# Kernel tuning notes

Measured on AMD Instinct MI355X. Metric: run time of the kernel, lower is better.

## Reference

```python
import jax, jax.numpy as jnp
import numpy as np

DIM = 512
HEADS = 8
DIM_HEAD = 64          # dim // 8
M = 256                # num_landmarks = dim // 2
PINV_ITERS = 6
SCALE = DIM_HEAD ** -0.5
KERNEL = 33            # residual_conv_kernel


def setup_inputs() -> dict:
    key = jax.random.key(0)
    ks = jax.random.split(key, 5)
    b, n = 4, 4096  # n divisible by M -> no padding branch
    inner = HEADS * DIM_HEAD
    x = jax.random.normal(ks[0], (b, n, DIM), jnp.float32)
    ln_w = jnp.ones((DIM,), jnp.float32)
    ln_b = jnp.zeros((DIM,), jnp.float32)
    w_qkv = jax.random.normal(ks[1], (DIM, 3 * inner), jnp.float32) / np.sqrt(DIM)
    w_out = jax.random.normal(ks[2], (inner, DIM), jnp.float32) / np.sqrt(inner)
    b_out = jnp.zeros((DIM,), jnp.float32)
    # depthwise Conv2d(heads, heads, (33,1), groups=heads, bias=False): weight [H,1,33,1]
    w_res = jax.random.normal(ks[3], (HEADS, 1, KERNEL, 1), jnp.float32) * 0.05
    return dict(x=x, ln_w=ln_w, ln_b=ln_b, w_qkv=w_qkv, w_out=w_out, b_out=b_out, w_res=w_res)


def moore_penrose_iter_pinv(x, iters=PINV_ITERS):
    # x: (..., m, m) row-stochastic softmax matrix
    abs_x = jnp.abs(x)
    col = abs_x.sum(-1).max()   # global max, matches torch.max(col)
    row = abs_x.sum(-2).max()
    z = jnp.swapaxes(x, -1, -2) / (col * row)
    I = jnp.eye(x.shape[-1], dtype=x.dtype)
    for _ in range(iters):
        xz = x @ z
        z = 0.25 * z @ (13 * I - xz @ (15 * I - xz @ (7 * I - xz)))
    return z


def reference(x, ln_w, ln_b, w_qkv, w_out, b_out, w_res):
    b, n, d = x.shape
    # pre-norm LayerNorm (eps=1e-5, biased variance)
    mu = x.mean(-1, keepdims=True)
    var = ((x - mu) ** 2).mean(-1, keepdims=True)
    h = (x - mu) * jax.lax.rsqrt(var + 1e-5) * ln_w + ln_b

    qkv = h @ w_qkv                           # (b, n, 3*inner)
    q, k, v = jnp.split(qkv, 3, axis=-1)
    to_heads = lambda t: t.reshape(b, n, HEADS, DIM_HEAD).transpose(0, 2, 1, 3)
    q = to_heads(q) * SCALE                   # (b, h, n, d)
    k = to_heads(k)
    v = to_heads(v)

    # landmarks: mean over consecutive chunks of size l = n // M
    l = n // M
    q_l = q.reshape(b, HEADS, M, l, DIM_HEAD).mean(3)  # (b, h, m, d)
    k_l = k.reshape(b, HEADS, M, l, DIM_HEAD).mean(3)

    sim1 = jnp.einsum('bhid,bhjd->bhij', q, k_l)       # (b, h, n, m)
    sim2 = jnp.einsum('bhid,bhjd->bhij', q_l, k_l)     # (b, h, m, m)
    sim3 = jnp.einsum('bhid,bhjd->bhij', q_l, k)       # (b, h, m, n)
    attn1 = jax.nn.softmax(sim1, -1)
    attn2 = jax.nn.softmax(sim2, -1)
    attn3 = jax.nn.softmax(sim3, -1)

    attn2_inv = moore_penrose_iter_pinv(attn2)
    out = (attn1 @ attn2_inv) @ (attn3 @ v)            # (b, h, n, d)

    # residual depthwise conv over sequence dim, per head
    pad = KERNEL // 2
    res = jax.lax.conv_general_dilated(
        v, w_res, window_strides=(1, 1), padding=((pad, pad), (0, 0)),
        dimension_numbers=('NCHW', 'OIHW', 'NCHW'), feature_group_count=HEADS)
    out = out + res

    out = out.transpose(0, 2, 1, 3).reshape(b, n, HEADS * DIM_HEAD)
    out = out @ w_out + b_out                          # to_out (dropout=identity in eval)
    return x + out
```

## Files before the change

kernel.cpp:

```cpp
#include <hip/hip_runtime.h>
#include <hip/hip_bf16.h>
#include <hip/hip_fp16.h>

#define B_ 4
#define H_ 8
#define N_ 4096
#define DH_ 64
#define D_ 512
#define M_ 256
#define BH_ 32
#define NT_ 16384

typedef unsigned short u16;
using sh8 = __attribute__((ext_vector_type(8))) short;
using sh4 = __attribute__((ext_vector_type(4))) short;
using f4  = __attribute__((ext_vector_type(4))) float;

__device__ __forceinline__ float bf2f(u16 u){ return __uint_as_float(((unsigned)u)<<16); }
__device__ __forceinline__ u16 f2bf(float f){
  unsigned u = __float_as_uint(f);
  u += 0x7fffu + ((u>>16)&1u);
  return (u16)(u>>16);
}

__global__ __launch_bounds__(256) void ln_kernel(const float* __restrict__ x,
    const float* __restrict__ w, const float* __restrict__ b, u16* __restrict__ h){
  int row = blockIdx.x;
  const float2* xr = (const float2*)(x + (size_t)row*D_);
  int t = threadIdx.x;
  float2 v = xr[t];
  float s = v.x+v.y, ss = v.x*v.x+v.y*v.y;
  #pragma unroll
  for (int o=32;o;o>>=1){ s += __shfl_xor(s,o); ss += __shfl_xor(ss,o); }
  __shared__ float sb[4], sb2[4];
  if ((t&63)==0){ sb[t>>6]=s; sb2[t>>6]=ss; }
  __syncthreads();
  float ts  = sb[0]+sb[1]+sb[2]+sb[3];
  float tss = sb2[0]+sb2[1]+sb2[2]+sb2[3];
  float mean = ts*(1.f/D_);
  float var  = tss*(1.f/D_) - mean*mean;
  float rstd = rsqrtf(var+1e-5f);
  int c = 2*t;
  float o0 = (v.x-mean)*rstd*w[c]   + b[c];
  float o1 = (v.y-mean)*rstd*w[c+1] + b[c+1];
  u16* hr = h + (size_t)row*D_;
  hr[c] = f2bf(o0); hr[c+1] = f2bf(o1);
}

__global__ void castT2_kernel(const float* __restrict__ wqkv, u16* __restrict__ wqkvT,
    const float* __restrict__ wout, u16* __restrict__ woutT){
  int idx = blockIdx.x*256 + threadIdx.x;
  if (idx < 512*1536){
    int k = idx/1536, n = idx - k*1536;
    wqkvT[(size_t)n*512 + k] = f2bf(wqkv[idx]);
  } else {
    int i2 = idx - 512*1536;
    if (i2 < 512*512){
      int k = i2>>9, n = i2&511;
      woutT[(size_t)n*512 + k] = f2bf(wout[i2]);
    }
  }
}

__global__ __launch_bounds__(256) void gemm_qkv(const u16* __restrict__ A,
    const u16* __restrict__ Bt, u16* __restrict__ q, u16* __restrict__ k, u16* __restrict__ v){
  __shared__ short As[128*72], Bs[128*72];
  int r0 = blockIdx.x*128, c0 = blockIdx.y*128;
  int tid = threadIdx.x, lane = tid&63, w = tid>>6;
  int wr = w>>1, wc = w&1;
  f4 acc[4][4];
  #pragma unroll
  for (int i=0;i<4;i++){
    #pragma unroll
    for (int j=0;j<4;j++) acc[i][j]=0;
  }
  for (int kt=0;kt<8;kt++){
    __syncthreads();
    #pragma unroll
    for (int i=0;i<4;i++){
      int c = i*256+tid, row = c>>3, kg = c&7;
      *(sh8*)&As[row*72+kg*8] = *(const sh8*)(A + (size_t)(r0+row)*512 + kt*64 + kg*8);
      *(sh8*)&Bs[row*72+kg*8] = *(const sh8*)(Bt + (size_t)(c0+row)*512 + kt*64 + kg*8);
    }
    __syncthreads();
    #pragma unroll
    for (int kc=0;kc<2;kc++){
      sh8 a[4], bq[4];
      #pragma unroll
      for (int fr=0;fr<4;fr++) a[fr]  = *(const sh8*)&As[(wr*64+fr*16+(lane&15))*72 + kc*32 + ((lane>>4)<<3)];
      #pragma unroll
      for (int fc=0;fc<4;fc++) bq[fc] = *(const sh8*)&Bs[(wc*64+fc*16+(lane&15))*72 + kc*32 + ((lane>>4)<<3)];
      #pragma unroll
      for (int fr=0;fr<4;fr++){
        #pragma unroll
        for (int fc=0;fc<4;fc++)
          acc[fr][fc] = __builtin_amdgcn_mfma_f32_16x16x32_bf16(a[fr], bq[fc], acc[fr][fc], 0,0,0);
      }
    }
  }
  #pragma unroll
  for (int fr=0;fr<4;fr++){
    #pragma unroll
    for (int fc=0;fc<4;fc++){
      #pragma unroll
      for (int j=0;j<4;j++){
        int r = r0 + wr*64 + fr*16 + ((lane>>4)<<2) + j;
        int c = c0 + wc*64 + fc*16 + (lane&15);
        float val = acc[fr][fc][j];
        int which = c>>9, hh = (c>>6)&7, d = c&63;
        int bb = r>>12, n = r&4095;
        if (which==0) val *= 0.125f;
        u16* dst = which==0 ? q : (which==1 ? k : v);
        dst[(((size_t)(bb*8+hh))*4096 + n)*64 + d] = f2bf(val);
      }
    }
  }
}

__global__ __launch_bounds__(64) void landmark_kernel(const u16* __restrict__ q,
    const u16* __restrict__ k, u16* __restrict__ ql, u16* __restrict__ kl){
  int bh = blockIdx.x, m = blockIdx.y, d = threadIdx.x;
  const u16* qp = q + (((size_t)bh*4096) + m*16)*64 + d;
  const u16* kp = k + (((size_t)bh*4096) + m*16)*64 + d;
  float sq=0, sk=0;
  #pragma unroll
  for (int j=0;j<16;j++){ sq += bf2f(qp[j*64]); sk += bf2f(kp[j*64]); }
  ql[((size_t)bh*256+m)*64+d] = f2bf(sq*(1.f/16.f));
  kl[((size_t)bh*256+m)*64+d] = f2bf(sk*(1.f/16.f));
}

__global__ __launch_bounds__(256) void attn2_kernel(const u16* __restrict__ ql,
    const u16* __restrict__ kl, u16* __restrict__ Xhi, u16* __restrict__ Xlo){
  int bh = blockIdx.x, rb = blockIdx.y;
  __shared__ short klds[256*72];
  const u16* kg = kl + (size_t)bh*256*64;
  int tid = threadIdx.x;
  #pragma unroll
  for (int i=0;i<8;i++){
    int c = i*256+tid, row = c>>3, kgi = c&7;
    *(sh8*)&klds[row*72+kgi*8] = *(const sh8*)(kg + row*64 + kgi*8);
  }
  __syncthreads();
  int r = rb*16 + (tid>>4), t = tid&15;
  const u16* qr = ql + ((size_t)bh*256 + r)*64;
  float qv[64];
  #pragma unroll
  for (int i=0;i<8;i++){
    sh8 v8 = *(const sh8*)(qr + i*8);
    #pragma unroll
    for (int j=0;j<8;j++) qv[i*8+j] = bf2f((u16)v8[j]);
  }
  float s[16];
  #pragma unroll
  for (int j=0;j<16;j++){
    int col = t + 16*j;
    const short* kr = &klds[col*72];
    float accv=0;
    #pragma unroll
    for (int i8=0;i8<8;i8++){
      sh8 kv = *(const sh8*)(kr + i8*8);
      #pragma unroll
      for (int jj=0;jj<8;jj++) accv += qv[i8*8+jj]*bf2f((u16)kv[jj]);
    }
    s[j]=accv;
  }
  float mx = s[0];
  #pragma unroll
  for (int j=1;j<16;j++) mx = fmaxf(mx, s[j]);
  #pragma unroll
  for (int o=1;o<16;o<<=1) mx = fmaxf(mx, __shfl_xor(mx,o));
  float sum=0;
  #pragma unroll
  for (int j=0;j<16;j++){ s[j] = __expf(s[j]-mx); sum += s[j]; }
  #pragma unroll
  for (int o=1;o<16;o<<=1) sum += __shfl_xor(sum,o);
  float inv = 1.f/sum;
  u16* Xh = Xhi + ((size_t)bh*256 + r)*256;
  u16* Xl = Xlo + ((size_t)bh*256 + r)*256;
  #pragma unroll
  for (int j=0;j<16;j++){
    float val = s[j]*inv;
    u16 hb = f2bf(val);
    Xh[t+16*j] = hb; Xl[t+16*j] = f2bf(val - bf2f(hb));
  }
}

__global__ __launch_bounds__(256) void colrow_kernel(const u16* __restrict__ Xhi,
    const u16* __restrict__ Xlo, float* __restrict__ scal){
  int bh = blockIdx.x, t = threadIdx.x;
  const u16* xh = Xhi + (size_t)bh*65536;
  const u16* xl = Xlo + (size_t)bh*65536;
  float cs=0, rs=0;
  for (int m=0;m<256;m++) cs += bf2f(xh[m*256+t]) + bf2f(xl[m*256+t]);
  for (int c=0;c<256;c++) rs += bf2f(xh[t*256+c]) + bf2f(xl[t*256+c]);
  #pragma unroll
  for (int o=32;o;o>>=1){ cs = fmaxf(cs, __shfl_xor(cs,o)); rs = fmaxf(rs, __shfl_xor(rs,o)); }
  __shared__ float sb[4], sb2[4];
  if ((t&63)==0){ sb[t>>6]=cs; sb2[t>>6]=rs; }
  __syncthreads();
  if (t==0){
    float mc = fmaxf(fmaxf(sb[0],sb[1]),fmaxf(sb[2],sb[3]));
    float mr = fmaxf(fmaxf(sb2[0],sb2[1]),fmaxf(sb2[2],sb2[3]));
    atomicMax((unsigned*)&scal[1], __float_as_uint(mc));
    atomicMax((unsigned*)&scal[0], __float_as_uint(mr));
  }
}

__global__ __launch_bounds__(256) void ztinit_kernel(const u16* __restrict__ Xhi,
    const u16* __restrict__ Xlo, const float* __restrict__ scal,
    u16* __restrict__ Zhi, u16* __restrict__ Zlo, u16* __restrict__ ZThi, u16* __restrict__ ZTlo){
  int bh = blockIdx.x; int xr0 = blockIdx.y*64, xc0 = blockIdx.z*64;
  __shared__ float tb[64*66];
  float inv = 1.f/(scal[0]*scal[1]);
  int tid = threadIdx.x;
  size_t mo = (size_t)bh*65536;
  int row = tid>>2, cof = (tid&3)*16;
  #pragma unroll
  for (int s2=0;s2<2;s2++){
    sh8 hv = *(const sh8*)(Xhi + mo + (size_t)(xr0+row)*256 + xc0+cof+s2*8);
    sh8 lv = *(const sh8*)(Xlo + mo + (size_t)(xr0+row)*256 + xc0+cof+s2*8);
    #pragma unroll
    for (int j=0;j<8;j++) tb[row*66 + cof+s2*8+j] = (bf2f((u16)hv[j])+bf2f((u16)lv[j]))*inv;
  }
  __syncthreads();
  int lc = tid&63;
  #pragma unroll
  for (int i=0;i<16;i++){
    int lr = i*4 + (tid>>6);
    float v1 = tb[lr*66+lc];
    u16 h1 = f2bf(v1);
    ZThi[mo + (size_t)(xr0+lr)*256 + xc0+lc] = h1;
    ZTlo[mo + (size_t)(xr0+lr)*256 + xc0+lc] = f2bf(v1 - bf2f(h1));
    float v2 = tb[lc*66+lr];
    u16 h2 = f2bf(v2);
    Zhi[mo + (size_t)(xc0+lr)*256 + xr0+lc] = h2;
    Zlo[mo + (size_t)(xc0+lr)*256 + xr0+lc] = f2bf(v2 - bf2f(h2));
  }
}

__global__ __launch_bounds__(256) void pinv_mm(
    const u16* __restrict__ Ahi, const u16* __restrict__ Alo,
    const u16* __restrict__ Bthi, const u16* __restrict__ Btlo,
    u16* __restrict__ Chi, u16* __restrict__ Clo,
    u16* __restrict__ CThi, u16* __restrict__ CTlo,
    float beta, float alpha, int mode){
  int bh = blockIdx.z, r0 = blockIdx.x*64, c0 = blockIdx.y*64;
  size_t mo = (size_t)bh*65536;
  __shared__ __align__(16) short smem[2][4*2560];
  int tid=threadIdx.x, lane=tid&63, w=tid>>6, wr=w>>1, wc=w&1;
  int srow = tid>>2, skof = (tid&3)*8;
  const u16* pA  = Ahi  + mo + (size_t)(r0+srow)*256 + skof;
  const u16* pAl = Alo  + mo + (size_t)(r0+srow)*256 + skof;
  const u16* pB  = Bthi + mo + (size_t)(c0+srow)*256 + skof;
  const u16* pBl = Btlo + mo + (size_t)(c0+srow)*256 + skof;
  float av[2][2][4];
  if (mode){
    #pragma unroll
    for (int fr=0;fr<2;fr++){
      #pragma unroll
      for (int fc=0;fc<2;fc++){
        #pragma unroll
        for (int j=0;j<4;j++){
          int lr = wr*32+fr*16+((lane>>4)<<2)+j, lc = wc*32+fc*16+(lane&15);
          size_t o = mo+(size_t)(r0+lr)*256+c0+lc;
          av[fr][fc][j] = bf2f(Ahi[o]) + bf2f(Alo[o]);
        }
      }
    }
  }
  sh8 ra  = *(const sh8*)(pA);
  sh8 ral = *(const sh8*)(pAl);
  sh8 rb  = *(const sh8*)(pB);
  sh8 rbl = *(const sh8*)(pBl);
  f4 acc[2][2];
  #pragma unroll
  for (int i=0;i<2;i++){
    #pragma unroll
    for (int j=0;j<2;j++) acc[i][j]=0;
  }
  for (int kt=0;kt<8;kt++){
    short* Ah = &smem[kt&1][0];
    short* Al = Ah + 2560; short* Bh = Ah + 5120; short* Bl = Ah + 7680;
    *(sh8*)&Ah[srow*40+skof] = ra;
    *(sh8*)&Al[srow*40+skof] = ral;
    *(sh8*)&Bh[srow*40+skof] = rb;
    *(sh8*)&Bl[srow*40+skof] = rbl;
    __syncthreads();
    if (kt<7){
      int o2 = (kt+1)*32;
      ra  = *(const sh8*)(pA+o2);  ral = *(const sh8*)(pAl+o2);
      rb  = *(const sh8*)(pB+o2);  rbl = *(const sh8*)(pBl+o2);
    }
    sh8 ah[2], al[2], bh8[2], bl8[2];
    #pragma unroll
    for (int fr=0;fr<2;fr++){
      int off = (wr*32+fr*16+(lane&15))*40 + ((lane>>4)<<3);
      ah[fr] = *(const sh8*)&Ah[off]; al[fr] = *(const sh8*)&Al[off];
    }
    #pragma unroll
    for (int fc=0;fc<2;fc++){
      int off = (wc*32+fc*16+(lane&15))*40 + ((lane>>4)<<3);
      bh8[fc] = *(const sh8*)&Bh[off]; bl8[fc] = *(const sh8*)&Bl[off];
    }
    #pragma unroll
    for (int fr=0;fr<2;fr++){
      #pragma unroll
      for (int fc=0;fc<2;fc++){
        acc[fr][fc] = __builtin_amdgcn_mfma_f32_16x16x32_bf16(ah[fr], bh8[fc], acc[fr][fc], 0,0,0);
        acc[fr][fc] = __builtin_amdgcn_mfma_f32_16x16x32_bf16(ah[fr], bl8[fc], acc[fr][fc], 0,0,0);
        acc[fr][fc] = __builtin_amdgcn_mfma_f32_16x16x32_bf16(al[fr], bh8[fc], acc[fr][fc], 0,0,0);
      }
    }
  }
  __syncthreads();
  float* tb = (float*)&smem[0][0];
  #pragma unroll
  for (int fr=0;fr<2;fr++){
    #pragma unroll
    for (int fc=0;fc<2;fc++){
      #pragma unroll
      for (int j=0;j<4;j++){
        int lr = wr*32+fr*16+((lane>>4)<<2)+j, lc = wc*32+fc*16+(lane&15);
        float val = acc[fr][fc][j];
        if (mode) val = alpha*(beta*av[fr][fc][j] - val);
        tb[lr*66+lc] = val;
      }
    }
  }
  __syncthreads();
  int lc2 = tid&63;
  #pragma unroll
  for (int i=0;i<16;i++){
    int lr2 = i*4+(tid>>6);
    if (Chi){
      float v1 = tb[lr2*66+lc2];
      u16 hb=f2bf(v1);
      Chi[mo+(size_t)(r0+lr2)*256+c0+lc2]=hb;
      Clo[mo+(size_t)(r0+lr2)*256+c0+lc2]=f2bf(v1-bf2f(hb));
    }
    if (CThi){
      float v2 = tb[lc2*66 + lr2];
      u16 hb2=f2bf(v2);
      CThi[mo+(size_t)(c0+lr2)*256 + r0+lc2]=hb2;
      CTlo[mo+(size_t)(c0+lr2)*256 + r0+lc2]=f2bf(v2-bf2f(hb2));
    }
  }
}

__global__ __launch_bounds__(256) void gemm_logits(const u16* __restrict__ Aall,
    const u16* __restrict__ Btall, __half* __restrict__ Oall,
    int N, size_t sA, size_t sB, size_t sO){
  int bh = blockIdx.z;
  const u16* A  = Aall  + (size_t)bh*sA + (size_t)blockIdx.x*128*64;
  const u16* Bt = Btall + (size_t)bh*sB + (size_t)blockIdx.y*128*64;
  __half* O = Oall + (size_t)bh*sO + (size_t)blockIdx.x*128*N + (size_t)blockIdx.y*128;
  __shared__ short As[128*72], Bs[128*72];
  int tid=threadIdx.x, lane=tid&63, w=tid>>6, wr=w>>1, wc=w&1;
  #pragma unroll
  for (int i=0;i<4;i++){
    int c=i*256+tid, row=c>>3, kg=c&7;
    *(sh8*)&As[row*72+kg*8] = *(const sh8*)(A  + (size_t)row*64 + kg*8);
    *(sh8*)&Bs[row*72+kg*8] = *(const sh8*)(Bt + (size_t)row*64 + kg*8);
  }
  __syncthreads();
  f4 acc[4][4];
  #pragma unroll
  for (int i=0;i<4;i++){
    #pragma unroll
    for (int j=0;j<4;j++) acc[i][j]=0;
  }
  #pragma unroll
  for (int kc=0;kc<2;kc++){
    sh8 a[4], bq[4];
    #pragma unroll
    for (int fr=0;fr<4;fr++) a[fr]  = *(const sh8*)&As[(wr*64+fr*16+(lane&15))*72 + kc*32 + ((lane>>4)<<3)];
    #pragma unroll
    for (int fc=0;fc<4;fc++) bq[fc] = *(const sh8*)&Bs[(wc*64+fc*16+(lane&15))*72 + kc*32 + ((lane>>4)<<3)];
    #pragma unroll
    for (int fr=0;fr<4;fr++){
      #pragma unroll
      for (int fc=0;fc<4;fc++)
        acc[fr][fc] = __builtin_amdgcn_mfma_f32_16x16x32_bf16(a[fr], bq[fc], acc[fr][fc], 0,0,0);
    }
  }
  #pragma unroll
  for (int fr=0;fr<4;fr++){
    #pragma unroll
    for (int fc=0;fc<4;fc++){
      #pragma unroll
      for (int j=0;j<4;j++)
        O[(size_t)(wr*64+fr*16+((lane>>4)<<2)+j)*N + wc*64+fc*16+(lane&15)] = __float2half(acc[fr][fc][j]);
    }
  }
}

__global__ __launch_bounds__(256) void stats_kernel(const __half* __restrict__ logits,
    float2* __restrict__ stats, int RL){
  size_t row = blockIdx.x;
  const __half2* p = (const __half2*)(logits + row*RL);
  int t = threadIdx.x, n2 = RL>>1;
  float mx = -1e30f;
  for (int i=t;i<n2;i+=256){ float2 f = __half22float2(p[i]); mx = fmaxf(mx, fmaxf(f.x,f.y)); }
  #pragma unroll
  for (int o=32;o;o>>=1) mx = fmaxf(mx, __shfl_xor(mx,o));
  __shared__ float sb[4], sb2[4];
  if ((t&63)==0) sb[t>>6]=mx;
  __syncthreads();
  mx = fmaxf(fmaxf(sb[0],sb[1]),fmaxf(sb[2],sb[3]));
  float s=0;
  for (int i=t;i<n2;i+=256){ float2 f = __half22float2(p[i]); s += __expf(f.x-mx)+__expf(f.y-mx); }
  #pragma unroll
  for (int o=32;o;o>>=1) s += __shfl_xor(s,o);
  if ((t&63)==0) sb2[t>>6]=s;
  __syncthreads();
  s = sb2[0]+sb2[1]+sb2[2]+sb2[3];
  if (t==0) stats[row] = make_float2(mx, 1.f/s);
}

__global__ __launch_bounds__(256) void gemm_out3(const __half* __restrict__ Lall,
    const float2* __restrict__ stall, const u16* __restrict__ vall, float* __restrict__ part){
  int bh = blockIdx.z, mt = blockIdx.x, ks = blockIdx.y;
  const __half* L = Lall + (size_t)bh*256*4096 + (size_t)mt*128*4096 + (size_t)ks*512;
  const float2* st = stall + (size_t)bh*256 + mt*128;
  const u16* V = vall + (size_t)bh*4096*64 + (size_t)ks*512*64;
  float* O = part + ((size_t)(bh*8+ks)*256 + (size_t)mt*128)*64;
  __shared__ short As[128*72], Bs[64*72];
  int tid=threadIdx.x, lane=tid&63, w=tid>>6;
  f4 acc[2][4];
  #pragma unroll
  for (int i=0;i<2;i++){
    #pragma unroll
    for (int j=0;j<4;j++) acc[i][j]=0;
  }
  for (int kt=0;kt<8;kt++){
    __syncthreads();
    #pragma unroll
    for (int i=0;i<4;i++){
      int c=i*256+tid, row=c>>3, kg=c&7;
      const __half2* src = (const __half2*)(L + (size_t)row*4096 + kt*64 + kg*8);
      float2 ms = st[row];
      sh8 ov;
      #pragma unroll
      for (int jj=0;jj<4;jj++){
        float2 f = __half22float2(src[jj]);
        ov[2*jj]   = (short)f2bf(__expf(f.x-ms.x)*ms.y);
        ov[2*jj+1] = (short)f2bf(__expf(f.y-ms.x)*ms.y);
      }
      *(sh8*)&As[row*72+kg*8] = ov;
    }
    #pragma unroll
    for (int i=0;i<16;i++){
      int c=i*256+tid, d=c&63, nl=c>>6;
      Bs[d*72+nl] = (short)V[(size_t)(kt*64+nl)*64 + d];
    }
    __syncthreads();
    #pragma unroll
    for (int kc=0;kc<2;kc++){
      sh8 a[2], bq[4];
      #pragma unroll
      for (int fr=0;fr<2;fr++) a[fr]  = *(const sh8*)&As[(w*32+fr*16+(lane&15))*72 + kc*32+((lane>>4)<<3)];
      #pragma unroll
      for (int fc=0;fc<4;fc++) bq[fc] = *(const sh8*)&Bs[(fc*16+(lane&15))*72 + kc*32+((lane>>4)<<3)];
      #pragma unroll
      for (int fr=0;fr<2;fr++){
        #pragma unroll
        for (int fc=0;fc<4;fc++)
          acc[fr][fc] = __builtin_amdgcn_mfma_f32_16x16x32_bf16(a[fr], bq[fc], acc[fr][fc], 0,0,0);
      }
    }
  }
  #pragma unroll
  for (int fr=0;fr<2;fr++){
    #pragma unroll
    for (int fc=0;fc<4;fc++){
      #pragma unroll
      for (int j=0;j<4;j++)
        O[(size_t)(w*32+fr*16+((lane>>4)<<2)+j)*64 + fc*16+(lane&15)] = acc[fr][fc][j];
    }
  }
}

__global__ __launch_bounds__(256) void reduce_o3(const float* __restrict__ part, float* __restrict__ o3){
  int idx = blockIdx.x*256+threadIdx.x;
  int bh = idx>>14, rem = idx & 16383;
  float s=0;
  #pragma unroll
  for (int ks=0;ks<8;ks++) s += part[(((size_t)(bh*8+ks))<<14) + rem];
  o3[idx]=s;
}

__global__ __launch_bounds__(256) void wt_kernel(const u16* __restrict__ Zhi,
    const u16* __restrict__ Zlo, const float* __restrict__ o3, u16* __restrict__ Wt){
  int bh = blockIdx.x; int m = blockIdx.y*4 + (threadIdx.x>>6); int d = threadIdx.x&63;
  const u16* zh = Zhi + ((size_t)bh*256 + m)*256;
  const u16* zl = Zlo + ((size_t)bh*256 + m)*256;
  const float* op = o3 + (size_t)bh*256*64 + d;
  float accv = 0;
  for (int kk=0;kk<256;kk++) accv += (bf2f(zh[kk])+bf2f(zl[kk]))*op[kk*64];
  Wt[((size_t)bh*64 + d)*256 + m] = f2bf(accv);
}

__global__ __launch_bounds__(256) void fused_out1(const u16* __restrict__ q,
    const u16* __restrict__ klall, const u16* __restrict__ Wtall, float* __restrict__ Oall){
  int rb = blockIdx.x, bh = blockIdx.y;
  __shared__ __align__(16) short sm[18432];
  short* Bs = sm; short* P = sm;
  int tid=threadIdx.x, lane=tid&63, w=tid>>6;
  const u16* qb  = q + ((size_t)bh*4096 + (size_t)rb*64)*64;
  const u16* klb = klall + (size_t)bh*256*64;
  const u16* Wt  = Wtall + (size_t)bh*64*256;
  #pragma unroll
  for (int i=0;i<8;i++){
    int c = i*256+tid, row = c>>3, kg = c&7;
    *(sh8*)&Bs[row*72+kg*8] = *(const sh8*)(klb + row*64 + kg*8);
  }
  const u16* qrow = qb + (size_t)(w*16+(lane&15))*64 + ((lane>>4)<<3);
  sh8 a0 = *(const sh8*)(qrow);
  sh8 a1 = *(const sh8*)(qrow + 32);
  __syncthreads();
  f4 acc[16];
  #pragma unroll
  for (int fc=0;fc<16;fc++){
    sh8 b0 = *(const sh8*)&Bs[(fc*16+(lane&15))*72 + ((lane>>4)<<3)];
    sh8 b1 = *(const sh8*)&Bs[(fc*16+(lane&15))*72 + 32 + ((lane>>4)<<3)];
    acc[fc]=0;
    acc[fc] = __builtin_amdgcn_mfma_f32_16x16x32_bf16(a0, b0, acc[fc], 0,0,0);
    acc[fc] = __builtin_amdgcn_mfma_f32_16x16x32_bf16(a1, b1, acc[fc], 0,0,0);
  }
  float inv_[4];
  #pragma unroll
  for (int j=0;j<4;j++){
    float mx=-1e30f;
    #pragma unroll
    for (int fc=0;fc<16;fc++) mx = fmaxf(mx, acc[fc][j]);
    #pragma unroll
    for (int o=1;o<16;o<<=1) mx = fmaxf(mx, __shfl_xor(mx,o));
    float s=0;
    #pragma unroll
    for (int fc=0;fc<16;fc++){ float e=__expf(acc[fc][j]-mx); acc[fc][j]=e; s+=e; }
    #pragma unroll
    for (int o=1;o<16;o<<=1) s += __shfl_xor(s,o);
    inv_[j] = 1.f/s;
  }
  __syncthreads();
  #pragma unroll
  for (int fc=0;fc<16;fc++){
    #pragma unroll
    for (int j=0;j<4;j++){
      int row = w*16 + ((lane>>4)<<2) + j, col = fc*16 + (lane&15);
      P[row*268 + col] = (short)f2bf(acc[fc][j]*inv_[j]);
    }
  }
  __syncthreads();
  f4 acc2[4];
  #pragma unroll
  for (int fc2=0;fc2<4;fc2++) acc2[fc2]=0;
  #pragma unroll
  for (int kc=0;kc<8;kc++){
    sh8 a = *(const sh8*)&P[(w*16+(lane&15))*268 + kc*32 + ((lane>>4)<<3)];
    #pragma unroll
    for (int fc2=0;fc2<4;fc2++){
      int d = fc2*16 + (lane&15);
      sh8 b = *(const sh8*)(Wt + (size_t)d*256 + (kc*4+(lane>>4))*8);
      acc2[fc2] = __builtin_amdgcn_mfma_f32_16x16x32_bf16(a, b, acc2[fc2], 0,0,0);
    }
  }
  float* O = Oall + ((size_t)bh*4096 + (size_t)rb*64)*64;
  #pragma unroll
  for (int fc2=0;fc2<4;fc2++){
    #pragma unroll
    for (int j=0;j<4;j++){
      int row = w*16 + ((lane>>4)<<2)+j, col = fc2*16+(lane&15);
      O[(size_t)row*64 + col] = acc2[fc2][j];
    }
  }
}

__global__ __launch_bounds__(256) void combine_kernel(const float* __restrict__ out1,
    const u16* __restrict__ v, const float* __restrict__ wres, u16* __restrict__ oc){
  int bh = blockIdx.x; int hh = bh&7, bb = bh>>3;
  int n0 = blockIdx.y*64;
  int tid = threadIdx.x, d = tid&63, sub = tid>>6;
  int nbase = n0 + sub*16;
  const u16* vb = v + ((size_t)bh*4096)*64 + d;
  float w_[33];
  #pragma unroll
  for (int j=0;j<33;j++) w_[j] = wres[hh*33+j];
  float vv[48];
  #pragma unroll
  for (int i=0;i<48;i++){
    int nn = nbase + i - 16;
    vv[i] = (nn>=0 && nn<4096) ? bf2f(vb[(size_t)nn*64]) : 0.f;
  }
  #pragma unroll
  for (int r=0;r<16;r++){
    int n = nbase + r;
    float acc = out1[(((size_t)bh*4096)+n)*64 + d];
    #pragma unroll
    for (int j=0;j<33;j++) acc += w_[j]*vv[r+j];
    oc[((size_t)(bb*4096+n))*512 + hh*64 + d] = f2bf(acc);
  }
}

__global__ __launch_bounds__(256) void gemm_final(const u16* __restrict__ A,
    const u16* __restrict__ Bt, const float* __restrict__ x, const float* __restrict__ bo,
    float* __restrict__ out){
  __shared__ short As[128*72], Bs[128*72];
  int r0 = blockIdx.x*128, c0 = blockIdx.y*128;
  int tid = threadIdx.x, lane = tid&63, w = tid>>6;
  int wr = w>>1, wc = w&1;
  f4 acc[4][4];
  #pragma unroll
  for (int i=0;i<4;i++){
    #pragma unroll
    for (int j=0;j<4;j++) acc[i][j]=0;
  }
  for (int kt=0;kt<8;kt++){
    __syncthreads();
    #pragma unroll
    for (int i=0;i<4;i++){
      int c = i*256+tid, row = c>>3, kg = c&7;
      *(sh8*)&As[row*72+kg*8] = *(const sh8*)(A  + (size_t)(r0+row)*512 + kt*64 + kg*8);
      *(sh8*)&Bs[row*72+kg*8] = *(const sh8*)(Bt + (size_t)(c0+row)*512 + kt*64 + kg*8);
    }
    __syncthreads();
    #pragma unroll
    for (int kc=0;kc<2;kc++){
      sh8 a[4], bq[4];
      #pragma unroll
      for (int fr=0;fr<4;fr++) a[fr]  = *(const sh8*)&As[(wr*64+fr*16+(lane&15))*72 + kc*32 + ((lane>>4)<<3)];
      #pragma unroll
      for (int fc=0;fc<4;fc++) bq[fc] = *(const sh8*)&Bs[(wc*64+fc*16+(lane&15))*72 + kc*32 + ((lane>>4)<<3)];
      #pragma unroll
      for (int fr=0;fr<4;fr++){
        #pragma unroll
        for (int fc=0;fc<4;fc++)
          acc[fr][fc] = __builtin_amdgcn_mfma_f32_16x16x32_bf16(a[fr], bq[fc], acc[fr][fc], 0,0,0);
      }
    }
  }
  #pragma unroll
  for (int fr=0;fr<4;fr++){
    #pragma unroll
    for (int fc=0;fc<4;fc++){
      #pragma unroll
      for (int j=0;j<4;j++){
        int r = r0 + wr*64 + fr*16 + ((lane>>4)<<2) + j;
        int c = c0 + wc*64 + fc*16 + (lane&15);
        out[(size_t)r*512+c] = x[(size_t)r*512+c] + acc[fr][fc][j] + bo[c];
      }
    }
  }
}

extern "C" void kernel_launch(void* const* d_in, const int* in_sizes, int n_in,
                              void* d_out, int out_size, void* d_ws, size_t ws_size,
                              hipStream_t stream){
  const float* x    = (const float*)d_in[0];
  const float* lnw  = (const float*)d_in[1];
  const float* lnb  = (const float*)d_in[2];
  const float* wqkv = (const float*)d_in[3];
  const float* wout = (const float*)d_in[4];
  const float* bout = (const float*)d_in[5];
  const float* wres = (const float*)d_in[6];
  float* out = (float*)d_out;

  char* ws = (char*)d_ws;
  size_t off = 0;
  auto alloc = [&](size_t bytes)->void*{ void* p = ws + off; off += (bytes + 255) & ~(size_t)255; return p; };
  u16* h      = (u16*)alloc((size_t)NT_*512*2);
  u16* wqkvT  = (u16*)alloc((size_t)1536*512*2);
  u16* woutT  = (u16*)alloc((size_t)512*512*2);
  u16* k      = (u16*)alloc((size_t)BH_*4096*64*2);
  u16* v      = (u16*)alloc((size_t)BH_*4096*64*2);
  u16* q      = (u16*)alloc((size_t)BH_*4096*64*2);
  float* part = (float*)alloc((size_t)BH_*8*256*64*4);
  u16* ql     = (u16*)alloc((size_t)BH_*256*64*2);
  u16* kl     = (u16*)alloc((size_t)BH_*256*64*2);
  u16* ZaChi  = (u16*)alloc((size_t)BH_*65536*2);
  u16* ZaClo  = (u16*)alloc((size_t)BH_*65536*2);
  __half* logits = (__half*)alloc((size_t)BH_*4096*256*2);
  float2* st3 = (float2*)alloc((size_t)BH_*256*8);
  float* o3   = (float*)alloc((size_t)BH_*256*64*4);
  u16* Wt     = (u16*)alloc((size_t)BH_*64*256*2);
  float* scal = (float*)alloc(256);
  float* out1 = (float*)logits;
  u16* oc     = h;

  const size_t C1 = (size_t)BH_*65536;
  u16* base = (u16*)logits;
  u16* Xhi  = base + 0*C1;  u16* Xlo  = base + 1*C1;
  u16* ZaThi= base + 2*C1;  u16* ZaTlo= base + 3*C1;
  u16* ZbChi= base + 4*C1;  u16* ZbClo= base + 5*C1;
  u16* ZbThi= base + 6*C1;  u16* ZbTlo= base + 7*C1;
  u16* T1Chi= base + 8*C1;  u16* T1Clo= base + 9*C1;
  u16* T1Thi= base +10*C1;  u16* T1Tlo= base +11*C1;
  u16* T2Thi= base +12*C1;  u16* T2Tlo= base +13*C1;
  u16* T3Thi= base +14*C1;  u16* T3Tlo= base +15*C1;

  ln_kernel<<<NT_, 256, 0, stream>>>(x, lnw, lnb, h);
  castT2_kernel<<<(512*1536+512*512+255)/256, 256, 0, stream>>>(wqkv, wqkvT, wout, woutT);
  gemm_qkv<<<dim3(128,12,1), 256, 0, stream>>>(h, wqkvT, q, k, v);
  landmark_kernel<<<dim3(32,256,1), 64, 0, stream>>>(q, k, ql, kl);
  attn2_kernel<<<dim3(32,16,1), 256, 0, stream>>>(ql, kl, Xhi, Xlo);
  hipMemsetAsync(scal, 0, 8, stream);
  colrow_kernel<<<32, 256, 0, stream>>>(Xhi, Xlo, scal);
  ztinit_kernel<<<dim3(32,4,4), 256, 0, stream>>>(Xhi, Xlo, scal, ZaChi, ZaClo, ZaThi, ZaTlo);

  u16 *zch=ZaChi, *zcl=ZaClo, *zth=ZaThi, *ztl=ZaTlo;
  u16 *wch=ZbChi, *wcl=ZbClo, *wth=ZbThi, *wtl=ZbTlo;
  for (int it=0; it<6; it++){
    pinv_mm<<<dim3(4,4,32),256,0,stream>>>(Xhi,Xlo, zth,ztl, T1Chi,T1Clo, T1Thi,T1Tlo, 0.f, 1.f, 0);
    pinv_mm<<<dim3(4,4,32),256,0,stream>>>(T1Chi,T1Clo, T1Thi,T1Tlo, (u16*)0,(u16*)0, T2Thi,T2Tlo, 7.f, 1.f, 1);
    pinv_mm<<<dim3(4,4,32),256,0,stream>>>(T1Chi,T1Clo, T2Thi,T2Tlo, (u16*)0,(u16*)0, T3Thi,T3Tlo, 15.f, 1.f, 1);
    pinv_mm<<<dim3(4,4,32),256,0,stream>>>(zch,zcl, T3Thi,T3Tlo, wch,wcl, wth,wtl, 13.f, 0.25f, 1);
    u16* t;
    t=zch; zch=wch; wch=t;  t=zcl; zcl=wcl; wcl=t;
    t=zth; zth=wth; wth=t;  t=ztl; ztl=wtl; wtl=t;
  }

  gemm_logits<<<dim3(2,32,32),256,0,stream>>>(ql, k, logits, 4096,
      (size_t)256*64, (size_t)4096*64, (size_t)256*4096);
  stats_kernel<<<BH_*256, 256, 0, stream>>>(logits, st3, 4096);
  gemm_out3<<<dim3(2,8,32),256,0,stream>>>(logits, st3, v, part);
  reduce_o3<<<2048, 256, 0, stream>>>(part, o3);
  wt_kernel<<<dim3(32,64,1),256,0,stream>>>(ZaChi, ZaClo, o3, Wt);
  fused_out1<<<dim3(64,32,1),256,0,stream>>>(q, kl, Wt, out1);
  combine_kernel<<<dim3(32,64,1),256,0,stream>>>(out1, v, wres, oc);
  gemm_final<<<dim3(128,4,1),256,0,stream>>>(oc, woutT, x, bout, out);
}
```

Baseline: 630.4 us.

## Restructure pinv iteration algebra, vectorize QKV epilogue, bf16 out1 intermediate

The Newton-Schulz pinv loop is reformulated so that XZ is carried forward: each iteration needs one square, one combined polynomial matmul with fused epilogue terms, and one batched launch that updates Z and the next XZ together. This cuts matmul launches and work per iteration from four to roughly three. The QKV GEMM epilogue now stages results through shared memory so it can write 16-byte vectorized bf16 stores. fused_out1 software-pipelines its Wt loads and writes out1 as bf16 instead of fp32, which halves that intermediate's traffic but adds rounding error.

```diff
diff --git a/kernel.cpp b/kernel.cpp
--- a/kernel.cpp
+++ b/kernel.cpp
@@ -64,7 +64,8 @@
 
 __global__ __launch_bounds__(256) void gemm_qkv(const u16* __restrict__ A,
     const u16* __restrict__ Bt, u16* __restrict__ q, u16* __restrict__ k, u16* __restrict__ v){
-  __shared__ short As[128*72], Bs[128*72];
+  __shared__ __align__(16) short sm[2*128*72];
+  short* As = sm; short* Bs = sm + 128*72;
   int r0 = blockIdx.x*128, c0 = blockIdx.y*128;
   int tid = threadIdx.x, lane = tid&63, w = tid>>6;
   int wr = w>>1, wc = w&1;
@@ -98,21 +99,36 @@
       }
     }
   }
-  #pragma unroll
-  for (int fr=0;fr<4;fr++){
-    #pragma unroll
-    for (int fc=0;fc<4;fc++){
-      #pragma unroll
-      for (int j=0;j<4;j++){
-        int r = r0 + wr*64 + fr*16 + ((lane>>4)<<2) + j;
-        int c = c0 + wc*64 + fc*16 + (lane&15);
-        float val = acc[fr][fc][j];
-        int which = c>>9, hh = (c>>6)&7, d = c&63;
-        int bb = r>>12, n = r&4095;
-        if (which==0) val *= 0.125f;
-        u16* dst = which==0 ? q : (which==1 ? k : v);
-        dst[(((size_t)(bb*8+hh))*4096 + n)*64 + d] = f2bf(val);
-      }
+  float* tb = (float*)sm;
+  #pragma unroll 1
+  for (int pass=0; pass<2; pass++){
+    __syncthreads();
+    if (wr==pass){
+      #pragma unroll
+      for (int fr=0;fr<4;fr++){
+        #pragma unroll
+        for (int fc=0;fc<4;fc++){
+          #pragma unroll
+          for (int j=0;j<4;j++)
+            tb[(fr*16+((lane>>4)<<2)+j)*132 + wc*64+fc*16+(lane&15)] = acc[fr][fc][j];
+        }
+      }
+    }
+    __syncthreads();
+    #pragma unroll
+    for (int i=0;i<4;i++){
+      int ch = i*256+tid;
+      int lr = ch>>4, cq = (ch&15)*8;
+      int r = r0 + pass*64 + lr;
+      int c = c0 + cq;
+      int which = c>>9, hh = (c>>6)&7, d = c&63;
+      int bb = r>>12, n = r&4095;
+      float scale = (which==0)? 0.125f : 1.f;
+      sh8 ov;
+      #pragma unroll
+      for (int jj=0;jj<8;jj++) ov[jj] = (short)f2bf(tb[lr*132+cq+jj]*scale);
+      u16* dst = which==0 ? q : (which==1 ? k : v);
+      *(sh8*)(dst + (((size_t)(bb*8+hh))*4096 + n)*64 + d) = ov;
     }
   }
 }
@@ -238,23 +254,24 @@
   }
 }
 
-__global__ __launch_bounds__(256) void pinv_mm(
+__device__ __forceinline__ void pinv_body(
     const u16* __restrict__ Ahi, const u16* __restrict__ Alo,
     const u16* __restrict__ Bthi, const u16* __restrict__ Btlo,
+    const u16* __restrict__ E1hi, const u16* __restrict__ E1lo,
+    const u16* __restrict__ E2hi, const u16* __restrict__ E2lo,
     u16* __restrict__ Chi, u16* __restrict__ Clo,
     u16* __restrict__ CThi, u16* __restrict__ CTlo,
-    float beta, float alpha, int mode){
-  int bh = blockIdx.z, r0 = blockIdx.x*64, c0 = blockIdx.y*64;
+    float k0, float k1, float k2, int bh, int r0, int col0,
+    short* smem){
   size_t mo = (size_t)bh*65536;
-  __shared__ __align__(16) short smem[2][4*2560];
   int tid=threadIdx.x, lane=tid&63, w=tid>>6, wr=w>>1, wc=w&1;
   int srow = tid>>2, skof = (tid&3)*8;
   const u16* pA  = Ahi  + mo + (size_t)(r0+srow)*256 + skof;
   const u16* pAl = Alo  + mo + (size_t)(r0+srow)*256 + skof;
-  const u16* pB  = Bthi + mo + (size_t)(c0+srow)*256 + skof;
-  const u16* pBl = Btlo + mo + (size_t)(c0+srow)*256 + skof;
-  float av[2][2][4];
-  if (mode){
+  const u16* pB  = Bthi + mo + (size_t)(col0+srow)*256 + skof;
+  const u16* pBl = Btlo + mo + (size_t)(col0+srow)*256 + skof;
+  float e1v[2][2][4], e2v[2][2][4];
+  if (E1hi){
     #pragma unroll
     for (int fr=0;fr<2;fr++){
       #pragma unroll
@@ -262,8 +279,22 @@
         #pragma unroll
         for (int j=0;j<4;j++){
           int lr = wr*32+fr*16+((lane>>4)<<2)+j, lc = wc*32+fc*16+(lane&15);
-          size_t o = mo+(size_t)(r0+lr)*256+c0+lc;
-          av[fr][fc][j] = bf2f(Ahi[o]) + bf2f(Alo[o]);
+          size_t o = mo+(size_t)(r0+lr)*256+col0+lc;
+          e1v[fr][fc][j] = bf2f(E1hi[o]) + bf2f(E1lo[o]);
+        }
+      }
+    }
+  }
+  if (E2hi){
+    #pragma unroll
+    for (int fr=0;fr<2;fr++){
+      #pragma unroll
+      for (int fc=0;fc<2;fc++){
+        #pragma unroll
+        for (int j=0;j<4;j++){
+          int lr = wr*32+fr*16+((lane>>4)<<2)+j, lc = wc*32+fc*16+(lane&15);
+          size_t o = mo+(size_t)(r0+lr)*256+col0+lc;
+          e2v[fr][fc][j] = bf2f(E2hi[o]) + bf2f(E2lo[o]);
         }
       }
     }
@@ -279,7 +310,7 @@
     for (int j=0;j<2;j++) acc[i][j]=0;
   }
   for (int kt=0;kt<8;kt++){
-    short* Ah = &smem[kt&1][0];
+    short* Ah = smem + (kt&1)*10240;
     short* Al = Ah + 2560; short* Bh = Ah + 5120; short* Bl = Ah + 7680;
     *(sh8*)&Ah[srow*40+skof] = ra;
     *(sh8*)&Al[srow*40+skof] = ral;
@@ -313,7 +344,7 @@
     }
   }
   __syncthreads();
-  float* tb = (float*)&smem[0][0];
+  float* tb = (float*)smem;
   #pragma unroll
   for (int fr=0;fr<2;fr++){
     #pragma unroll
@@ -321,8 +352,9 @@
       #pragma unroll
       for (int j=0;j<4;j++){
         int lr = wr*32+fr*16+((lane>>4)<<2)+j, lc = wc*32+fc*16+(lane&15);
-        float val = acc[fr][fc][j];
-        if (mode) val = alpha*(beta*av[fr][fc][j] - val);
+        float val = k0*acc[fr][fc][j];
+        if (E1hi) val += k1*e1v[fr][fc][j];
+        if (E2hi) val += k2*e2v[fr][fc][j];
         tb[lr*66+lc] = val;
       }
     }
@@ -335,16 +367,43 @@
     if (Chi){
       float v1 = tb[lr2*66+lc2];
       u16 hb=f2bf(v1);
-      Chi[mo+(size_t)(r0+lr2)*256+c0+lc2]=hb;
-      Clo[mo+(size_t)(r0+lr2)*256+c0+lc2]=f2bf(v1-bf2f(hb));
+      Chi[mo+(size_t)(r0+lr2)*256+col0+lc2]=hb;
+      Clo[mo+(size_t)(r0+lr2)*256+col0+lc2]=f2bf(v1-bf2f(hb));
     }
     if (CThi){
       float v2 = tb[lc2*66 + lr2];
       u16 hb2=f2bf(v2);
-      CThi[mo+(size_t)(c0+lr2)*256 + r0+lc2]=hb2;
-      CTlo[mo+(size_t)(c0+lr2)*256 + r0+lc2]=f2bf(v2-bf2f(hb2));
-    }
-  }
+      CThi[mo+(size_t)(col0+lr2)*256 + r0+lc2]=hb2;
+      CTlo[mo+(size_t)(col0+lr2)*256 + r0+lc2]=f2bf(v2-bf2f(hb2));
+    }
+  }
+}
+
+__global__ __launch_bounds__(256) void pinv_mm(
+    const u16* Ahi, const u16* Alo, const u16* Bthi, const u16* Btlo,
+    const u16* E1hi, const u16* E1lo, const u16* E2hi, const u16* E2lo,
+    u16* Chi, u16* Clo, u16* CThi, u16* CTlo,
+    float k0, float k1, float k2){
+  __shared__ __align__(16) short smem[2*10240];
+  pinv_body(Ahi,Alo,Bthi,Btlo,E1hi,E1lo,E2hi,E2lo,Chi,Clo,CThi,CTlo,
+            k0,k1,k2, blockIdx.z, blockIdx.x*64, blockIdx.y*64, smem);
+}
+
+__global__ __launch_bounds__(256) void pinv_zupd(
+    const u16* Zhi, const u16* Zlo, u16* ZnHi, u16* ZnLo,
+    const u16* T1hi, const u16* T1lo,
+    u16* TnChi, u16* TnClo, u16* TnThi, u16* TnTlo,
+    const u16* Bthi, const u16* Btlo){
+  __shared__ __align__(16) short smem[2*10240];
+  int which = blockIdx.z >> 5, bh = blockIdx.z & 31;
+  const u16* Ah = which ? T1hi : Zhi;
+  const u16* Al = which ? T1lo : Zlo;
+  u16* Ch  = which ? TnChi : ZnHi;
+  u16* Cl  = which ? TnClo : ZnLo;
+  u16* CTh = which ? TnThi : (u16*)0;
+  u16* CTl = which ? TnTlo : (u16*)0;
+  pinv_body(Ah,Al,Bthi,Btlo, Ah,Al, (u16*)0,(u16*)0, Ch,Cl,CTh,CTl,
+            -0.25f, 3.25f, 0.f, bh, blockIdx.x*64, blockIdx.y*64, smem);
 }
 
 __global__ __launch_bounds__(256) void gemm_logits(const u16* __restrict__ Aall,
@@ -501,7 +560,7 @@
 }
 
 __global__ __launch_bounds__(256) void fused_out1(const u16* __restrict__ q,
-    const u16* __restrict__ klall, const u16* __restrict__ Wtall, float* __restrict__ Oall){
+    const u16* __restrict__ klall, const u16* __restrict__ Wtall, u16* __restrict__ Oall){
   int rb = blockIdx.x, bh = blockIdx.y;
   __shared__ __align__(16) short sm[18432];
   short* Bs = sm; short* P = sm;
@@ -555,28 +614,55 @@
   f4 acc2[4];
   #pragma unroll
   for (int fc2=0;fc2<4;fc2++) acc2[fc2]=0;
-  #pragma unroll
-  for (int kc=0;kc<8;kc++){
-    sh8 a = *(const sh8*)&P[(w*16+(lane&15))*268 + kc*32 + ((lane>>4)<<3)];
+  sh8 bqA[4], bqB[4];
+  #pragma unroll
+  for (int fc2=0;fc2<4;fc2++){
+    int d = fc2*16 + (lane&15);
+    bqA[fc2] = *(const sh8*)(Wt + (size_t)d*256 + ((lane>>4))*8);
+  }
+  #pragma unroll
+  for (int kp=0;kp<4;kp++){
+    int kc0 = kp*2, kc1 = kp*2+1;
     #pragma unroll
     for (int fc2=0;fc2<4;fc2++){
       int d = fc2*16 + (lane&15);
-      sh8 b = *(const sh8*)(Wt + (size_t)d*256 + (kc*4+(lane>>4))*8);
-      acc2[fc2] = __builtin_amdgcn_mfma_f32_16x16x32_bf16(a, b, acc2[fc2], 0,0,0);
-    }
-  }
-  float* O = Oall + ((size_t)bh*4096 + (size_t)rb*64)*64;
+      bqB[fc2] = *(const sh8*)(Wt + (size_t)d*256 + (kc1*4+(lane>>4))*8);
+    }
+    sh8 a = *(const sh8*)&P[(w*16+(lane&15))*268 + kc0*32 + ((lane>>4)<<3)];
+    #pragma unroll
+    for (int fc2=0;fc2<4;fc2++)
+      acc2[fc2] = __builtin_amdgcn_mfma_f32_16x16x32_bf16(a, bqA[fc2], acc2[fc2], 0,0,0);
+    if (kp<3){
+      #pragma unroll
+      for (int fc2=0;fc2<4;fc2++){
+        int d = fc2*16 + (lane&15);
+        bqA[fc2] = *(const sh8*)(Wt + (size_t)d*256 + ((kc1+1)*4+(lane>>4))*8);
+      }
+    }
+    sh8 a2 = *(const sh8*)&P[(w*16+(lane&15))*268 + kc1*32 + ((lane>>4)<<3)];
+    #pragma unroll
+    for (int fc2=0;fc2<4;fc2++)
+      acc2[fc2] = __builtin_amdgcn_mfma_f32_16x16x32_bf16(a2, bqB[fc2], acc2[fc2], 0,0,0);
+  }
+  __syncthreads();
+  u16* otb = (u16*)sm;
   #pragma unroll
   for (int fc2=0;fc2<4;fc2++){
     #pragma unroll
-    for (int j=0;j<4;j++){
-      int row = w*16 + ((lane>>4)<<2)+j, col = fc2*16+(lane&15);
-      O[(size_t)row*64 + col] = acc2[fc2][j];
-    }
-  }
-}
-
-__global__ __launch_bounds__(256) void combine_kernel(const float* __restrict__ out1,
+    for (int j=0;j<4;j++)
+      otb[(w*16+((lane>>4)<<2)+j)*72 + fc2*16+(lane&15)] = f2bf(acc2[fc2][j]);
+  }
+  __syncthreads();
+  u16* O = Oall + ((size_t)bh*4096 + (size_t)rb*64)*64;
+  #pragma unroll
+  for (int i=0;i<2;i++){
+    int ch = i*256+tid; int lr = ch>>3, cq = (ch&7)*8;
+    sh8 ov = *(sh8*)&otb[lr*72+cq];
+    *(sh8*)(O + (size_t)lr*64 + cq) = ov;
+  }
+}
+
+__global__ __launch_bounds__(256) void combine_kernel(const u16* __restrict__ out1,
     const u16* __restrict__ v, const float* __restrict__ wres, u16* __restrict__ oc){
   int bh = blockIdx.x; int hh = bh&7, bb = bh>>3;
   int n0 = blockIdx.y*64;
@@ -595,7 +681,7 @@
   #pragma unroll
   for (int r=0;r<16;r++){
     int n = nbase + r;
-    float acc = out1[(((size_t)bh*4096)+n)*64 + d];
+    float acc = bf2f(out1[(((size_t)bh*4096)+n)*64 + d]);
     #pragma unroll
     for (int j=0;j<33;j++) acc += w_[j]*vv[r+j];
     oc[((size_t)(bb*4096+n))*512 + hh*64 + d] = f2bf(acc);
@@ -679,24 +765,27 @@
   u16* kl     = (u16*)alloc((size_t)BH_*256*64*2);
   u16* ZaChi  = (u16*)alloc((size_t)BH_*65536*2);
   u16* ZaClo  = (u16*)alloc((size_t)BH_*65536*2);
+  u16* ZbChi  = (u16*)alloc((size_t)BH_*65536*2);
+  u16* ZbClo  = (u16*)alloc((size_t)BH_*65536*2);
   __half* logits = (__half*)alloc((size_t)BH_*4096*256*2);
   float2* st3 = (float2*)alloc((size_t)BH_*256*8);
   float* o3   = (float*)alloc((size_t)BH_*256*64*4);
   u16* Wt     = (u16*)alloc((size_t)BH_*64*256*2);
   float* scal = (float*)alloc(256);
-  float* out1 = (float*)logits;
+  u16* out1   = (u16*)logits;
   u16* oc     = h;
 
   const size_t C1 = (size_t)BH_*65536;
   u16* base = (u16*)logits;
-  u16* Xhi  = base + 0*C1;  u16* Xlo  = base + 1*C1;
-  u16* ZaThi= base + 2*C1;  u16* ZaTlo= base + 3*C1;
-  u16* ZbChi= base + 4*C1;  u16* ZbClo= base + 5*C1;
-  u16* ZbThi= base + 6*C1;  u16* ZbTlo= base + 7*C1;
-  u16* T1Chi= base + 8*C1;  u16* T1Clo= base + 9*C1;
-  u16* T1Thi= base +10*C1;  u16* T1Tlo= base +11*C1;
-  u16* T2Thi= base +12*C1;  u16* T2Tlo= base +13*C1;
-  u16* T3Thi= base +14*C1;  u16* T3Tlo= base +15*C1;
+  u16* Xhi   = base + 0*C1;  u16* Xlo   = base + 1*C1;
+  u16* T1aCh = base + 2*C1;  u16* T1aCl = base + 3*C1;
+  u16* T1aTh = base + 4*C1;  u16* T1aTl = base + 5*C1;
+  u16* T1bCh = base + 6*C1;  u16* T1bCl = base + 7*C1;
+  u16* T1bTh = base + 8*C1;  u16* T1bTl = base + 9*C1;
+  u16* SCh   = base +10*C1;  u16* SCl   = base +11*C1;
+  u16* STh   = base +12*C1;  u16* STl   = base +13*C1;
+  u16* T3h   = base +14*C1;  u16* T3l   = base +15*C1;
+  u16* Z0Th  = SCh;          u16* Z0Tl  = SCl;
 
   ln_kernel<<<NT_, 256, 0, stream>>>(x, lnw, lnb, h);
   castT2_kernel<<<(512*1536+512*512+255)/256, 256, 0, stream>>>(wqkv, wqkvT, wout, woutT);
@@ -705,18 +794,30 @@
   attn2_kernel<<<dim3(32,16,1), 256, 0, stream>>>(ql, kl, Xhi, Xlo);
   hipMemsetAsync(scal, 0, 8, stream);
   colrow_kernel<<<32, 256, 0, stream>>>(Xhi, Xlo, scal);
-  ztinit_kernel<<<dim3(32,4,4), 256, 0, stream>>>(Xhi, Xlo, scal, ZaChi, ZaClo, ZaThi, ZaTlo);
-
-  u16 *zch=ZaChi, *zcl=ZaClo, *zth=ZaThi, *ztl=ZaTlo;
-  u16 *wch=ZbChi, *wcl=ZbClo, *wth=ZbThi, *wtl=ZbTlo;
+  ztinit_kernel<<<dim3(32,4,4), 256, 0, stream>>>(Xhi, Xlo, scal, ZaChi, ZaClo, Z0Th, Z0Tl);
+
+  u16* nul = (u16*)0;
+  pinv_mm<<<dim3(4,4,32),256,0,stream>>>(Xhi,Xlo, Z0Th,Z0Tl, nul,nul,nul,nul,
+      T1aCh,T1aCl, T1aTh,T1aTl, 1.f,0.f,0.f);
+  u16 *TcCh=T1aCh,*TcCl=T1aCl,*TcTh=T1aTh,*TcTl=T1aTl;
+  u16 *TnCh=T1bCh,*TnCl=T1bCl,*TnTh=T1bTh,*TnTl=T1bTl;
+  u16 *Zch=ZaChi,*Zcl=ZaClo, *Znh=ZbChi,*Znl=ZbClo;
   for (int it=0; it<6; it++){
-    pinv_mm<<<dim3(4,4,32),256,0,stream>>>(Xhi,Xlo, zth,ztl, T1Chi,T1Clo, T1Thi,T1Tlo, 0.f, 1.f, 0);
-    pinv_mm<<<dim3(4,4,32),256,0,stream>>>(T1Chi,T1Clo, T1Thi,T1Tlo, (u16*)0,(u16*)0, T2Thi,T2Tlo, 7.f, 1.f, 1);
-    pinv_mm<<<dim3(4,4,32),256,0,stream>>>(T1Chi,T1Clo, T2Thi,T2Tlo, (u16*)0,(u16*)0, T3Thi,T3Tlo, 15.f, 1.f, 1);
-    pinv_mm<<<dim3(4,4,32),256,0,stream>>>(zch,zcl, T3Thi,T3Tlo, wch,wcl, wth,wtl, 13.f, 0.25f, 1);
-    u16* t;
-    t=zch; zch=wch; wch=t;  t=zcl; zcl=wcl; wcl=t;
-    t=zth; zth=wth; wth=t;  t=ztl; ztl=wtl; wtl=t;
+    pinv_mm<<<dim3(4,4,32),256,0,stream>>>(TcCh,TcCl, TcTh,TcTl, nul,nul,nul,nul,
+        SCh,SCl, STh,STl, 1.f,0.f,0.f);
+    pinv_mm<<<dim3(4,4,32),256,0,stream>>>(TcCh,TcCl, STh,STl, TcCh,TcCl, SCh,SCl,
+        nul,nul, T3h,T3l, 1.f,15.f,-7.f);
+    if (it<5){
+      pinv_zupd<<<dim3(4,4,64),256,0,stream>>>(Zch,Zcl, Znh,Znl,
+          TcCh,TcCl, TnCh,TnCl, TnTh,TnTl, T3h,T3l);
+      u16* t;
+      t=Zch;Zch=Znh;Znh=t; t=Zcl;Zcl=Znl;Znl=t;
+      t=TcCh;TcCh=TnCh;TnCh=t; t=TcCl;TcCl=TnCl;TnCl=t;
+      t=TcTh;TcTh=TnTh;TnTh=t; t=TcTl;TcTl=TnTl;TnTl=t;
+    } else {
+      pinv_mm<<<dim3(4,4,32),256,0,stream>>>(Zch,Zcl, T3h,T3l, Zch,Zcl, nul,nul,
+          Znh,Znl, nul,nul, -0.25f,3.25f,0.f);
+    }
   }
 
   gemm_logits<<<dim3(2,32,32),256,0,stream>>>(ql, k, logits, 4096,
```

Result: faster. 611.4 us (-3.0%).
